# Optimization experiments

Measured on AMD Instinct MI355X. Metric: run time of the kernel, lower is better.

The kernel has to match this reference:

```python
import jax, jax.numpy as jnp
import numpy as np

NC, S, T, F, D, A = 617, 200000, 15, 5, 64, 768
E, EC, L = 1000000, 20000, 2


def setup_inputs():
    key = jax.random.key(0)
    ks = jax.random.split(key, 24)
    f = jnp.float32
    sc = 0.08
    return {
        "company_ts": jax.random.normal(ks[0], (NC, T, F), f),
        "sentence_x": jax.random.normal(ks[1], (S, A), f),
        "company_ids": jnp.arange(NC, dtype=jnp.int32),
        "ei_c2c_src": jax.random.randint(ks[2], (EC,), 0, NC),
        "ei_c2c_dst": jax.random.randint(ks[3], (EC,), 0, NC),
        "ei_s2c_src": jax.random.randint(ks[4], (E,), 0, S),
        "ei_s2c_dst": jax.random.randint(ks[5], (E,), 0, NC),
        "ei_c2s_src": jax.random.randint(ks[6], (E,), 0, NC),
        "ei_c2s_dst": jax.random.randint(ks[7], (E,), 0, S),
        "bn_gamma": jnp.ones((T,), f),
        "bn_beta": jnp.zeros((T,), f),
        "lstm_Wih0": sc * jax.random.normal(ks[8], (4 * D, 1), f),
        "lstm_Whh0": sc * jax.random.normal(ks[9], (4 * D, D), f),
        "lstm_bih0": jnp.zeros((4 * D,), f),
        "lstm_bhh0": jnp.zeros((4 * D,), f),
        "lstm_Wih1": sc * jax.random.normal(ks[10], (4 * D, D), f),
        "lstm_Whh1": sc * jax.random.normal(ks[11], (4 * D, D), f),
        "lstm_bih1": jnp.zeros((4 * D,), f),
        "lstm_bhh1": jnp.zeros((4 * D,), f),
        "fc_W": sc * jax.random.normal(ks[12], (D, D), f),
        "fc_b": jnp.zeros((D,), f),
        "comp_emb": jax.random.normal(ks[13], (NC, D), f),
        "proj_W": sc * jax.random.normal(ks[14], (D, A), f),
        "proj_b": jnp.zeros((D,), f),
        "gin_W": sc * jax.random.normal(ks[15], (L, 3, D, D), f),
        "gin_b": jnp.zeros((L, 3, D), f),
        "gin_a": 0.25 * jnp.ones((L, 3), f),  # PReLU slope, torch default init
        "cls_W": sc * jax.random.normal(ks[16], (2, D), f),
        "cls_b": jnp.zeros((2,), f),
    }


def _lstm_layer(x, Wih, Whh, bih, bhh):
    # x: [N, T, I] -> [N, T, H]; torch gate order i, f, g, o
    N = x.shape[0]
    H = Whh.shape[1]

    def step(carry, xt):
        h, c = carry
        g = xt @ Wih.T + h @ Whh.T + bih + bhh
        i, fg, gg, o = jnp.split(g, 4, axis=-1)
        c = jax.nn.sigmoid(fg) * c + jax.nn.sigmoid(i) * jnp.tanh(gg)
        h = jax.nn.sigmoid(o) * jnp.tanh(c)
        return (h, c), h

    init = (jnp.zeros((N, H), x.dtype), jnp.zeros((N, H), x.dtype))
    _, hs = jax.lax.scan(step, init, jnp.swapaxes(x, 0, 1))
    return jnp.swapaxes(hs, 0, 1)


def _gin(x_src, x_dst, src, dst, n_dst, W, b, a):
    # GINConv(eps=0), nn = Linear + PReLU: prelu(W @ (x_dst + sum_{e->i} x_src[src_e]) + b)
    msg = jax.ops.segment_sum(x_src[src], dst, num_segments=n_dst)
    h = (x_dst + msg) @ W.T + b
    return jnp.where(h >= 0, h, a * h)


def reference(company_ts, sentence_x, company_ids, ei_c2c_src, ei_c2c_dst,
              ei_s2c_src, ei_s2c_dst, ei_c2s_src, ei_c2s_dst,
              bn_gamma, bn_beta, lstm_Wih0, lstm_Whh0, lstm_bih0, lstm_bhh0,
              lstm_Wih1, lstm_Whh1, lstm_bih1, lstm_bhh1, fc_W, fc_b,
              comp_emb, proj_W, proj_b, gin_W, gin_b, gin_a, cls_W, cls_b):
    # LSTM branch on the second-to-last timeseries feature
    ts = company_ts[:, :, -2:-1]                       # [NC, T, 1]
    mean = ts.mean(axis=(0, 2), keepdims=True)         # BatchNorm1d(T), training stats
    var = ts.var(axis=(0, 2), keepdims=True)
    ts = (ts - mean) / jnp.sqrt(var + 1e-5)
    ts = ts * bn_gamma[None, :, None] + bn_beta[None, :, None]
    h = _lstm_layer(ts, lstm_Wih0, lstm_Whh0, lstm_bih0, lstm_bhh0)
    h = _lstm_layer(h, lstm_Wih1, lstm_Whh1, lstm_bih1, lstm_bhh1)
    comp_ts = jax.nn.relu(h[:, -1, :] @ fc_W.T + fc_b)  # [NC, D]

    # node features: company = lstm + embedding; sentence = projected article emb
    comp = comp_ts + comp_emb[company_ids]
    sent = sentence_x @ proj_W.T + proj_b               # [S, D]

    # to_hetero(GConv): per-edge-type GINConv, sum-aggregate over edge types per dst type
    n_comp, n_sent = comp.shape[0], sent.shape[0]
    for l in range(gin_W.shape[0]):
        new_comp = (_gin(comp, comp, ei_c2c_src, ei_c2c_dst, n_comp,
                         gin_W[l, 0], gin_b[l, 0], gin_a[l, 0])
                    + _gin(sent, comp, ei_s2c_src, ei_s2c_dst, n_comp,
                           gin_W[l, 1], gin_b[l, 1], gin_a[l, 1]))
        new_sent = _gin(comp, sent, ei_c2s_src, ei_c2s_dst, n_sent,
                        gin_W[l, 2], gin_b[l, 2], gin_a[l, 2])
        comp, sent = new_comp, new_sent

    return comp @ cls_W.T + cls_b                       # [NC, 2]
```

## Files before the change

kernel.cpp:

```cpp
#include <hip/hip_runtime.h>

#define NCC 617
#define TTT 15
#define FFF 5
#define SSN 200000
#define EEN 1000000
#define ECN 20000
#define CSBLK 196
#define NB2 512
#define EPB2 ((EEN + NB2 - 1) / NB2)
#define ZN (NCC + NCC + SSN + SSN)
#define HALLB ((ECN + EEN + 255) / 256)

typedef unsigned short u16;
typedef unsigned int   u32;

using short8  = __attribute__((ext_vector_type(8))) short;
using f32x4v  = __attribute__((ext_vector_type(4))) float;

__device__ __forceinline__ float bf2f(u16 u){ return __uint_as_float(((u32)u) << 16); }
__device__ __forceinline__ u16 f2bf(float f){
  u32 x = __float_as_uint(f);
  u32 r = (x + 0x7fffu + ((x >> 16) & 1u)) >> 16;
  return (u16)r;
}
__device__ __forceinline__ u32 pk2(float a, float b){ return (u32)f2bf(a) | ((u32)f2bf(b) << 16); }
__device__ __forceinline__ float sigm(float x){ return 1.0f / (1.0f + __expf(-x)); }

__global__ __launch_bounds__(256) void k_zero(int* p, int n){
  int i = blockIdx.x * 256 + threadIdx.x;
  if (i < n) p[i] = 0;
}

__global__ __launch_bounds__(256) void k_histF(const int* __restrict__ s2c_dst, int* __restrict__ blockHist,
                                               const int* __restrict__ c2c_dst, int* __restrict__ cnt_c2c,
                                               const int* __restrict__ c2s_dst, int* __restrict__ cnt_c2s){
  __shared__ int h[NCC];
  int b = blockIdx.x, tid = threadIdx.x;
  if (b < NB2){
    for (int i = tid; i < NCC; i += 256) h[i] = 0;
    __syncthreads();
    int e0 = b * EPB2;
    int e1 = e0 + EPB2; if (e1 > EEN) e1 = EEN;
    for (int e = e0 + tid; e < e1; e += 256) atomicAdd(&h[s2c_dst[e]], 1);
    __syncthreads();
    for (int i = tid; i < NCC; i += 256) blockHist[i * NB2 + b] = h[i];
  } else {
    int i = (b - NB2) * 256 + tid;
    if (i < ECN) atomicAdd(&cnt_c2c[c2c_dst[i]], 1);
    else if (i < ECN + EEN) atomicAdd(&cnt_c2s[c2s_dst[i - ECN]], 1);
  }
}

__global__ __launch_bounds__(1024) void k_scanA(int* __restrict__ blockHist, int* __restrict__ colTotal,
                                                const int* __restrict__ cnt_c2s, int* __restrict__ off_c2s,
                                                int* __restrict__ bsum,
                                                const float* __restrict__ ts, const float* __restrict__ gamma,
                                                const float* __restrict__ beta, float* __restrict__ tsn){
  __shared__ int buf[1024];
  __shared__ float ss[1024], s2[1024];
  int b = blockIdx.x, tid = threadIdx.x;
  if (b < NCC){
    if (tid < 64){
      int lane = tid;
      int base = 0;
      for (int j = 0; j < NB2; j += 64){
        int v = blockHist[b * NB2 + j + lane];
        int orig = v;
        #pragma unroll
        for (int s = 1; s < 64; s <<= 1){
          int t = __shfl_up(v, s, 64);
          if (lane >= s) v += t;
        }
        blockHist[b * NB2 + j + lane] = base + v - orig;
        base += __shfl(v, 63, 64);
      }
      if (lane == 0) colTotal[b] = base;
    }
  } else if (b < NCC + CSBLK) {
    int bb = b - NCC;
    int gi = bb * 1024 + tid;
    int v = (gi < SSN) ? cnt_c2s[gi] : 0;
    buf[tid] = v;
    __syncthreads();
    for (int d = 1; d < 1024; d <<= 1){
      int x = (tid >= d) ? buf[tid - d] : 0;
      __syncthreads();
      buf[tid] += x;
      __syncthreads();
    }
    if (gi < SSN) off_c2s[gi] = buf[tid] - v;
    if (tid == 1023) bsum[bb] = buf[1023];
  } else {
    int t = b - (NCC + CSBLK);
    float a = 0.f, s = 0.f;
    for (int c = tid; c < NCC; c += 1024){
      float v = ts[(c * TTT + t) * FFF + 3];
      a += v; s += v * v;
    }
    ss[tid] = a; s2[tid] = s;
    __syncthreads();
    for (int d = 512; d > 0; d >>= 1){
      if (tid < d){ ss[tid] += ss[tid + d]; s2[tid] += s2[tid + d]; }
      __syncthreads();
    }
    float mean = ss[0] / (float)NCC;
    float var  = s2[0] / (float)NCC - mean * mean;
    float rstd = rsqrtf(var + 1e-5f);
    float g = gamma[t], be = beta[t];
    for (int c = tid; c < NCC; c += 1024){
      float v = ts[(c * TTT + t) * FFF + 3];
      tsn[c * TTT + t] = (v - mean) * rstd * g + be;
    }
  }
}

__global__ __launch_bounds__(1024) void k_scanB(const int* __restrict__ cnt_c2c, int* __restrict__ off_c2c,
                                                const int* __restrict__ colTotal, int* __restrict__ off_s2c,
                                                int* __restrict__ off_c2s, const int* __restrict__ bsum){
  __shared__ int buf[1024];
  __shared__ int sboff[CSBLK + 1];
  int b = blockIdx.x, tid = threadIdx.x;
  if (b == 0){
    for (int pass = 0; pass < 2; ++pass){
      const int* cnt = pass ? colTotal : cnt_c2c;
      int* ofs = pass ? off_s2c : off_c2c;
      int v = (tid < NCC) ? cnt[tid] : 0;
      buf[tid] = v;
      __syncthreads();
      for (int d = 1; d < 1024; d <<= 1){
        int x = (tid >= d) ? buf[tid - d] : 0;
        __syncthreads();
        buf[tid] += x;
        __syncthreads();
      }
      if (tid < NCC) ofs[tid] = (tid == 0) ? 0 : buf[tid - 1];
      if (tid == 0) ofs[NCC] = buf[NCC - 1];
      __syncthreads();
    }
  } else {
    int bb = b - 1;
    int lane = tid & 63;
    if (tid < 64){
      int base = 0;
      for (int j = 0; j < CSBLK; j += 64){
        int idx = j + lane;
        int v = (idx < CSBLK) ? bsum[idx] : 0;
        int orig = v;
        #pragma unroll
        for (int s = 1; s < 64; s <<= 1){
          int t2 = __shfl_up(v, s, 64);
          if (lane >= s) v += t2;
        }
        if (idx < CSBLK) sboff[idx] = base + v - orig;
        base += __shfl(v, 63, 64);
      }
      if (lane == 0) sboff[CSBLK] = base;
    }
    __syncthreads();
    int gi = bb * 1024 + tid;
    if (gi < SSN) off_c2s[gi] += sboff[bb];
    if (bb == 0 && tid == 0) off_c2s[SSN] = sboff[CSBLK];
  }
}

__global__ __launch_bounds__(256) void k_scatF(const int* __restrict__ s2c_src, const int* __restrict__ s2c_dst,
                                               const int* __restrict__ blockHist, const int* __restrict__ off_s2c,
                                               int* __restrict__ bkt_s2c,
                                               const int* __restrict__ c2c_src, const int* __restrict__ c2c_dst,
                                               const int* __restrict__ off_c2c, int* __restrict__ cnt2_c2c,
                                               int* __restrict__ bkt_c2c,
                                               const int* __restrict__ c2s_src, const int* __restrict__ c2s_dst,
                                               const int* __restrict__ off_c2s, int* __restrict__ cnt2_c2s,
                                               int* __restrict__ bkt_c2s){
  __shared__ int cur[NCC];
  int b = blockIdx.x, tid = threadIdx.x;
  if (b < NB2){
    for (int i = tid; i < NCC; i += 256) cur[i] = off_s2c[i] + blockHist[i * NB2 + b];
    __syncthreads();
    int e0 = b * EPB2;
    int e1 = e0 + EPB2; if (e1 > EEN) e1 = EEN;
    for (int e = e0 + tid; e < e1; e += 256){
      int d = s2c_dst[e];
      int p = atomicAdd(&cur[d], 1);
      bkt_s2c[p] = s2c_src[e];
    }
  } else {
    int i = (b - NB2) * 256 + tid;
    if (i < ECN){
      int d = c2c_dst[i]; int p = off_c2c[d] + atomicAdd(&cnt2_c2c[d], 1); bkt_c2c[p] = c2c_src[i];
    } else if (i < ECN + EEN){
      int k = i - ECN;
      int d = c2s_dst[k]; int p = off_c2s[d] + atomicAdd(&cnt2_c2s[d], 1); bkt_c2s[p] = c2s_src[k];
    }
  }
}

__global__ __launch_bounds__(256, 1) void k_lstm01(const float* __restrict__ tsn,
                                                   const float* __restrict__ Wih0, const float* __restrict__ Whh0,
                                                   const float* __restrict__ bih0, const float* __restrict__ bhh0,
                                                   const float* __restrict__ Wih1, const float* __restrict__ Whh1,
                                                   const float* __restrict__ bih1, const float* __restrict__ bhh1,
                                                   const float* __restrict__ fcW, const float* __restrict__ fcb,
                                                   const float* __restrict__ emb, const int* __restrict__ ids,
                                                   float* __restrict__ comp0){
  __shared__ __align__(16) u16 sW0[64 * 64 * 4];
  __shared__ __align__(16) u16 sP1[64 * 64 * 8];
  __shared__ float sWi[256];
  __shared__ float sB0[256];
  int tid = threadIdx.x;
  for (int i = tid; i < 16384; i += 256){
    int k = i >> 8, j = (i >> 2) & 63, g = i & 3;
    sW0[i] = f2bf(Whh0[(g * 64 + j) * 64 + k]);
  }
  for (int i = tid; i < 32768; i += 256){
    int k = i >> 9, j = (i >> 3) & 63, g = i & 7;
    float v = (g < 4) ? Wih1[(g * 64 + j) * 64 + k] : Whh1[((g - 4) * 64 + j) * 64 + k];
    sP1[i] = f2bf(v);
  }
  sWi[tid] = Wih0[tid];
  sB0[tid] = bih0[tid] + bhh0[tid];
  __syncthreads();
  int wave = tid >> 6, lane = tid & 63;
  int c = blockIdx.x * 4 + wave;
  int ci = (c < NCC) ? c : (NCC - 1);
  float wi_i = sWi[lane], wi_f = sWi[64 + lane], wi_g = sWi[128 + lane], wi_o = sWi[192 + lane];
  float b0i = sB0[lane], b0f = sB0[64 + lane], b0g = sB0[128 + lane], b0o = sB0[192 + lane];
  float b1i = bih1[lane]       + bhh1[lane];
  float b1f = bih1[64 + lane]  + bhh1[64 + lane];
  float b1g = bih1[128 + lane] + bhh1[128 + lane];
  float b1o = bih1[192 + lane] + bhh1[192 + lane];
  float h0 = 0.f, c0 = 0.f, h1 = 0.f, c1 = 0.f;
  for (int t = 0; t < TTT; ++t){
    float x = tsn[ci * TTT + t];
    float gi = b0i + x * wi_i, gf = b0f + x * wi_f, gg = b0g + x * wi_g, go = b0o + x * wi_o;
    #pragma unroll 4
    for (int k = 0; k < 64; ++k){
      float hk = __shfl(h0, k, 64);
      ushort4 w = *(const ushort4*)&sW0[(k * 64 + lane) * 4];
      gi += hk * bf2f(w.x); gf += hk * bf2f(w.y);
      gg += hk * bf2f(w.z); go += hk * bf2f(w.w);
    }
    c0 = sigm(gf) * c0 + sigm(gi) * tanhf(gg);
    h0 = sigm(go) * tanhf(c0);
    gi = b1i; gf = b1f; gg = b1g; go = b1o;
    #pragma unroll 4
    for (int k = 0; k < 64; ++k){
      float xk = __shfl(h0, k, 64);
      float hk = __shfl(h1, k, 64);
      short8 wv = *(const short8*)&sP1[(k * 64 + lane) * 8];
      gi += xk * bf2f((u16)wv[0]) + hk * bf2f((u16)wv[4]);
      gf += xk * bf2f((u16)wv[1]) + hk * bf2f((u16)wv[5]);
      gg += xk * bf2f((u16)wv[2]) + hk * bf2f((u16)wv[6]);
      go += xk * bf2f((u16)wv[3]) + hk * bf2f((u16)wv[7]);
    }
    c1 = sigm(gf) * c1 + sigm(gi) * tanhf(gg);
    h1 = sigm(go) * tanhf(c1);
  }
  __syncthreads();
  float* fws = (float*)sW0;
  for (int i = tid; i < 4096; i += 256){
    int d = i >> 6, k = i & 63;
    fws[k * 64 + d] = fcW[i];
  }
  __syncthreads();
  float y = fcb[lane];
  #pragma unroll 4
  for (int k = 0; k < 64; ++k){
    float hk = __shfl(h1, k, 64);
    y += hk * fws[k * 64 + lane];
  }
  y = fmaxf(y, 0.f);
  if (c < NCC) comp0[c * 64 + lane] = y + emb[ids[c] * 64 + lane];
}

__global__ __launch_bounds__(256) void k_projm(const float* __restrict__ A, const float* __restrict__ W,
                                               const float* __restrict__ pb, u16* __restrict__ sent0){
  __shared__ __align__(16) u16 sA[128 * 64];
  __shared__ __align__(16) u16 sB[64 * 64];
  char* sAb = (char*)sA;
  char* sBb = (char*)sB;
  int tid = threadIdx.x;
  int wave = tid >> 6, lane = tid & 63;
  int l15 = lane & 15, lg = lane >> 4;
  int s0 = blockIdx.x * 128;

  int rA = tid >> 1, hA = tid & 1;
  int sA_row = s0 + rA; if (sA_row >= SSN) sA_row = SSN - 1;
  const float* gA0 = &A[(size_t)sA_row * 768 + hA * 32];
  u32 aw_base = (u32)(rA * 128 + hA * 64);
  u32 aw_swz  = (u32)((rA & 7) << 4);
  int nB = tid >> 2, qB = tid & 3;
  const float* gB0 = &W[(size_t)nB * 768 + qB * 16];
  u32 bw_base = (u32)(nB * 128 + qB * 32);
  u32 bw_swz  = (u32)((nB & 7) << 4);

  int arow = wave * 32 + l15;
  u32 ar_swz = (u32)((arow & 7) << 4);
  u32 ar_base = (u32)(arow * 128 + lg * 16);
  u32 br_swz = (u32)((l15 & 7) << 4);
  u32 br_base = (u32)(l15 * 128 + lg * 16);

  f32x4v acc[2][4] = {};

  for (int kc = 0; kc < 12; ++kc){
    __syncthreads();
    {
      const float* g = gA0 + kc * 64;
      #pragma unroll
      for (int q = 0; q < 4; ++q){
        float4 va = ((const float4*)g)[2 * q];
        float4 vb = ((const float4*)g)[2 * q + 1];
        uint4 w;
        w.x = pk2(va.x, va.y); w.y = pk2(va.z, va.w);
        w.z = pk2(vb.x, vb.y); w.w = pk2(vb.z, vb.w);
        *(uint4*)(sAb + ((aw_base + q * 16) ^ aw_swz)) = w;
      }
    }
    {
      const float* g = gB0 + kc * 64;
      #pragma unroll
      for (int q = 0; q < 2; ++q){
        float4 va = ((const float4*)g)[2 * q];
        float4 vb = ((const float4*)g)[2 * q + 1];
        uint4 w;
        w.x = pk2(va.x, va.y); w.y = pk2(va.z, va.w);
        w.z = pk2(vb.x, vb.y); w.w = pk2(vb.z, vb.w);
        *(uint4*)(sBb + ((bw_base + q * 16) ^ bw_swz)) = w;
      }
    }
    __syncthreads();
    #pragma unroll
    for (int ks = 0; ks < 2; ++ks){
      short8 a0 = *(const short8*)(sAb + ((ar_base + 0    + ks * 64) ^ ar_swz));
      short8 a1 = *(const short8*)(sAb + ((ar_base + 2048 + ks * 64) ^ ar_swz));
      short8 b0 = *(const short8*)(sBb + ((br_base + 0    + ks * 64) ^ br_swz));
      short8 b1 = *(const short8*)(sBb + ((br_base + 2048 + ks * 64) ^ br_swz));
      short8 b2 = *(const short8*)(sBb + ((br_base + 4096 + ks * 64) ^ br_swz));
      short8 b3 = *(const short8*)(sBb + ((br_base + 6144 + ks * 64) ^ br_swz));
      acc[0][0] = __builtin_amdgcn_mfma_f32_16x16x32_bf16(a0, b0, acc[0][0], 0, 0, 0);
      acc[0][1] = __builtin_amdgcn_mfma_f32_16x16x32_bf16(a0, b1, acc[0][1], 0, 0, 0);
      acc[0][2] = __builtin_amdgcn_mfma_f32_16x16x32_bf16(a0, b2, acc[0][2], 0, 0, 0);
      acc[0][3] = __builtin_amdgcn_mfma_f32_16x16x32_bf16(a0, b3, acc[0][3], 0, 0, 0);
      acc[1][0] = __builtin_amdgcn_mfma_f32_16x16x32_bf16(a1, b0, acc[1][0], 0, 0, 0);
      acc[1][1] = __builtin_amdgcn_mfma_f32_16x16x32_bf16(a1, b1, acc[1][1], 0, 0, 0);
      acc[1][2] = __builtin_amdgcn_mfma_f32_16x16x32_bf16(a1, b2, acc[1][2], 0, 0, 0);
      acc[1][3] = __builtin_amdgcn_mfma_f32_16x16x32_bf16(a1, b3, acc[1][3], 0, 0, 0);
    }
  }

  float bias[4];
  #pragma unroll
  for (int nt = 0; nt < 4; ++nt) bias[nt] = pb[nt * 16 + l15];
  #pragma unroll
  for (int mt = 0; mt < 2; ++mt){
    #pragma unroll
    for (int j = 0; j < 4; ++j){
      int s = s0 + wave * 32 + mt * 16 + lg * 4 + j;
      if (s < SSN){
        #pragma unroll
        for (int nt = 0; nt < 4; ++nt)
          sent0[(size_t)s * 64 + nt * 16 + l15] = f2bf(acc[mt][nt][j] + bias[nt]);
      }
    }
  }
}

__global__ __launch_bounds__(256) void k_sgin(const u16* __restrict__ sentIn, const float* __restrict__ compIn,
                                              const int* __restrict__ ofs, const int* __restrict__ bkt,
                                              const float* __restrict__ W, const float* __restrict__ b,
                                              const float* __restrict__ aP, u16* __restrict__ sentOut){
  __shared__ __align__(16) u16 sX[64 * 64];
  __shared__ __align__(16) u16 sW[64 * 64];
  __shared__ int eb[512];
  __shared__ int sofs[65];
  char* sXb = (char*)sX;
  char* sWb = (char*)sW;
  int tid = threadIdx.x;
  {
    int n = tid >> 2, q = tid & 3;
    const float* g = &W[n * 64 + q * 16];
    u32 wbase = (u32)(n * 128 + q * 32);
    u32 wswz  = (u32)((n & 7) << 4);
    #pragma unroll
    for (int hh = 0; hh < 2; ++hh){
      float4 va = ((const float4*)g)[2 * hh];
      float4 vb = ((const float4*)g)[2 * hh + 1];
      uint4 w;
      w.x = pk2(va.x, va.y); w.y = pk2(va.z, va.w);
      w.z = pk2(vb.x, vb.y); w.w = pk2(vb.z, vb.w);
      *(uint4*)(sWb + ((wbase + hh * 16) ^ wswz)) = w;
    }
  }
  int sBase = blockIdx.x * 64;
  if (tid < 65) sofs[tid] = ofs[sBase + tid];
  __syncthreads();
  int E0 = sofs[0];
  int tot = sofs[64] - E0;
  int staged = tot < 512 ? tot : 512;
  for (int i = tid; i < staged; i += 256) eb[i] = bkt[E0 + i];
  __syncthreads();
  int wave = tid >> 6, lane = tid & 63;
  for (int q = 0; q < 16; ++q){
    int sL = wave * 16 + q;
    int s = sBase + sL;
    float acc = bf2f(sentIn[(size_t)s * 64 + lane]);
    int e0 = sofs[sL], e1 = sofs[sL + 1];
    for (int e = e0; e < e1; ++e){
      int r = e - E0;
      int src = (r < 512) ? eb[r] : bkt[e];
      acc += compIn[src * 64 + lane];
    }
    *(u16*)(sXb + (((u32)(sL * 128 + lane * 2)) ^ ((u32)((sL & 7) << 4)))) = f2bf(acc);
  }
  __syncthreads();
  int l15 = lane & 15, lg = lane >> 4;
  int arow = wave * 16 + l15;
  u32 ar_swz = (u32)((arow & 7) << 4);
  u32 br_swz = (u32)((l15 & 7) << 4);
  f32x4v acc4[4] = {};
  #pragma unroll
  for (int ks = 0; ks < 2; ++ks){
    short8 a0 = *(const short8*)(sXb + (((u32)(arow * 128 + ks * 64 + lg * 16)) ^ ar_swz));
    #pragma unroll
    for (int nt = 0; nt < 4; ++nt){
      short8 b0 = *(const short8*)(sWb + (((u32)((nt * 16 + l15) * 128 + ks * 64 + lg * 16)) ^ br_swz));
      acc4[nt] = __builtin_amdgcn_mfma_f32_16x16x32_bf16(a0, b0, acc4[nt], 0, 0, 0);
    }
  }
  float alpha = *aP;
  #pragma unroll
  for (int nt = 0; nt < 4; ++nt){
    float bb = b[nt * 16 + l15];
    #pragma unroll
    for (int j = 0; j < 4; ++j){
      int srow = sBase + wave * 16 + lg * 4 + j;
      float h = acc4[nt][j] + bb;
      h = (h >= 0.f) ? h : alpha * h;
      sentOut[(size_t)srow * 64 + nt * 16 + l15] = f2bf(h);
    }
  }
}

__global__ __launch_bounds__(1024) void k_cgin(const float* __restrict__ compIn, const u16* __restrict__ sentIn,
                                               const int* __restrict__ ofsA, const int* __restrict__ bktA,
                                               const int* __restrict__ ofsB, const int* __restrict__ bktB,
                                               const float* __restrict__ Wa, const float* __restrict__ ba, const float* aaP,
                                               const float* __restrict__ Wb, const float* __restrict__ bb, const float* abP,
                                               float* __restrict__ compOut,
                                               const float* __restrict__ clsW, const float* __restrict__ clsb,
                                               float* __restrict__ outp){
  __shared__ __align__(16) float Wat[64 * 68];
  __shared__ __align__(16) float Wbt[64 * 68];
  __shared__ int eidx[2048];
  __shared__ float part[16][2][64];
  __shared__ float xa[64], xb[64], outab[128];
  int tid = threadIdx.x;
  for (int i = tid; i < 4096; i += 1024){
    int j = i >> 6, k = i & 63;
    Wat[k * 68 + j] = Wa[i];
    Wbt[k * 68 + j] = Wb[i];
  }
  int wave = tid >> 6, lane = tid & 63;
  int c = blockIdx.x;
  float accA = 0.f, accB = 0.f;
  int a0 = ofsA[c], a1 = ofsA[c + 1];
  for (int base = a0; base < a1; base += 2048){
    int cnt = a1 - base; if (cnt > 2048) cnt = 2048;
    __syncthreads();
    for (int i = tid; i < cnt; i += 1024) eidx[i] = bktA[base + i];
    __syncthreads();
    for (int i = wave; i < cnt; i += 16) accA += compIn[eidx[i] * 64 + lane];
  }
  int b0 = ofsB[c], b1 = ofsB[c + 1];
  for (int base = b0; base < b1; base += 2048){
    int cnt = b1 - base; if (cnt > 2048) cnt = 2048;
    __syncthreads();
    for (int i = tid; i < cnt; i += 1024) eidx[i] = bktB[base + i];
    __syncthreads();
    #pragma unroll 4
    for (int i = wave; i < cnt; i += 16) accB += bf2f(sentIn[(size_t)eidx[i] * 64 + lane]);
  }
  part[wave][0][lane] = accA;
  part[wave][1][lane] = accB;
  __syncthreads();
  if (tid < 128){
    int l = tid & 63, which = tid >> 6;
    float m = 0.f;
    #pragma unroll
    for (int w = 0; w < 16; ++w) m += part[w][which][l];
    float ci = compIn[c * 64 + l];
    if (which == 0) xa[l] = ci + m; else xb[l] = ci + m;
  }
  __syncthreads();
  if (tid < 128){
    int j = tid & 63;
    const float* X  = (tid < 64) ? xa : xb;
    const float* Wt = (tid < 64) ? Wat : Wbt;
    float acc = (tid < 64) ? ba[j] : bb[j];
    #pragma unroll 4
    for (int k = 0; k < 64; ++k) acc += X[k] * Wt[k * 68 + j];
    float al = (tid < 64) ? *aaP : *abP;
    outab[tid] = (acc >= 0.f) ? acc : al * acc;
  }
  __syncthreads();
  if (clsW){
    if (tid < 64) xa[tid] = outab[tid] + outab[64 + tid];
    __syncthreads();
    if (tid < 128){
      int j = tid >> 6;
      float p = xa[lane] * clsW[j * 64 + lane];
      #pragma unroll
      for (int s = 32; s > 0; s >>= 1) p += __shfl_down(p, s, 64);
      if (lane == 0) outp[c * 2 + j] = p + clsb[j];
    }
  } else {
    if (tid < 64) compOut[c * 64 + tid] = outab[tid] + outab[64 + tid];
  }
}

extern "C" void kernel_launch(void* const* d_in, const int* in_sizes, int n_in,
                              void* d_out, int out_size, void* d_ws, size_t ws_size,
                              hipStream_t stream) {
  (void)in_sizes; (void)n_in; (void)out_size; (void)ws_size;
  const float* company_ts = (const float*)d_in[0];
  const float* sentence_x = (const float*)d_in[1];
  const int*   company_ids = (const int*)d_in[2];
  const int*   c2c_src = (const int*)d_in[3];
  const int*   c2c_dst = (const int*)d_in[4];
  const int*   s2c_src = (const int*)d_in[5];
  const int*   s2c_dst = (const int*)d_in[6];
  const int*   c2s_src = (const int*)d_in[7];
  const int*   c2s_dst = (const int*)d_in[8];
  const float* bn_gamma = (const float*)d_in[9];
  const float* bn_beta  = (const float*)d_in[10];
  const float* Wih0 = (const float*)d_in[11];
  const float* Whh0 = (const float*)d_in[12];
  const float* bih0 = (const float*)d_in[13];
  const float* bhh0 = (const float*)d_in[14];
  const float* Wih1 = (const float*)d_in[15];
  const float* Whh1 = (const float*)d_in[16];
  const float* bih1 = (const float*)d_in[17];
  const float* bhh1 = (const float*)d_in[18];
  const float* fc_W = (const float*)d_in[19];
  const float* fc_b = (const float*)d_in[20];
  const float* comp_emb = (const float*)d_in[21];
  const float* proj_W = (const float*)d_in[22];
  const float* proj_b = (const float*)d_in[23];
  const float* gin_W = (const float*)d_in[24];
  const float* gin_b = (const float*)d_in[25];
  const float* gin_a = (const float*)d_in[26];
  const float* cls_W = (const float*)d_in[27];
  const float* cls_b = (const float*)d_in[28];
  float* outp = (float*)d_out;

  char* ws = (char*)d_ws;
  size_t off = 0;
  auto alloc = [&](size_t bytes)->char* {
    char* r = ws + off;
    off += (bytes + 255) & ~(size_t)255;
    return r;
  };
  float* ts_norm = (float*)alloc((size_t)NCC * TTT * 4);
  float* comp0   = (float*)alloc((size_t)NCC * 64 * 4);
  float* comp1   = (float*)alloc((size_t)NCC * 64 * 4);
  u16*   sent0   = (u16*)alloc((size_t)SSN * 64 * 2);
  int*   blockHist = (int*)alloc((size_t)NCC * NB2 * 4);
  int*   colTotal  = (int*)alloc((size_t)NCC * 4);
  int*   cnt_c2c  = (int*)alloc((size_t)ZN * 4);
  int*   cnt2_c2c = cnt_c2c + NCC;
  int*   cnt_c2s  = cnt2_c2c + NCC;
  int*   cnt2_c2s = cnt_c2s + SSN;
  int*   off_c2c = (int*)alloc((size_t)(NCC + 1) * 4);
  int*   off_s2c = (int*)alloc((size_t)(NCC + 1) * 4);
  int*   off_c2s = (int*)alloc((size_t)(SSN + 1) * 4);
  int*   bkt_c2c = (int*)alloc((size_t)ECN * 4);
  int*   bkt_s2c = (int*)alloc((size_t)EEN * 4);
  int*   bkt_c2s = (int*)alloc((size_t)EEN * 4);
  int*   bsum    = (int*)alloc(256 * 4);

  k_zero<<<(ZN + 255) / 256, 256, 0, stream>>>(cnt_c2c, ZN);
  k_histF<<<NB2 + HALLB, 256, 0, stream>>>(s2c_dst, blockHist, c2c_dst, cnt_c2c, c2s_dst, cnt_c2s);
  k_scanA<<<NCC + CSBLK + TTT, 1024, 0, stream>>>(blockHist, colTotal, cnt_c2s, off_c2s, bsum,
                                                  company_ts, bn_gamma, bn_beta, ts_norm);
  k_scanB<<<1 + CSBLK, 1024, 0, stream>>>(cnt_c2c, off_c2c, colTotal, off_s2c, off_c2s, bsum);
  k_scatF<<<NB2 + HALLB, 256, 0, stream>>>(s2c_src, s2c_dst, blockHist, off_s2c, bkt_s2c,
                                           c2c_src, c2c_dst, off_c2c, cnt2_c2c, bkt_c2c,
                                           c2s_src, c2s_dst, off_c2s, cnt2_c2s, bkt_c2s);

  k_lstm01<<<(NCC + 3) / 4, 256, 0, stream>>>(ts_norm, Wih0, Whh0, bih0, bhh0,
                                              Wih1, Whh1, bih1, bhh1,
                                              fc_W, fc_b, comp_emb, company_ids, comp0);

  k_projm<<<(SSN + 127) / 128, 256, 0, stream>>>(sentence_x, proj_W, proj_b, sent0);

  k_cgin<<<NCC, 1024, 0, stream>>>(comp0, sent0,
                                   off_c2c, bkt_c2c, off_s2c, bkt_s2c,
                                   gin_W + 0 * 4096, gin_b + 0 * 64, gin_a + 0,
                                   gin_W + 1 * 4096, gin_b + 1 * 64, gin_a + 1,
                                   comp1, nullptr, nullptr, nullptr);
  k_sgin<<<SSN / 64, 256, 0, stream>>>(sent0, comp0, off_c2s, bkt_c2s,
                                       gin_W + 2 * 4096, gin_b + 2 * 64, gin_a + 2,
                                       sent0 );

  k_cgin<<<NCC, 1024, 0, stream>>>(comp1, sent0,
                                   off_c2c, bkt_c2c, off_s2c, bkt_s2c,
                                   gin_W + 3 * 4096, gin_b + 3 * 64, gin_a + 3,
                                   gin_W + 4 * 4096, gin_b + 4 * 64, gin_a + 4,
                                   nullptr, cls_W, cls_b, outp);
}
```

Measured before the change: 565.3 us.

## Fuse layer-0 company and sentence GIN into one launch with separate output buffer

Merges the layer-0 company GIN and sentence GIN kernels into a single launch, where the first blocks handle companies and the rest handle sentences in 256-row tiles of 1024 threads. Sentence output now goes to a new sent1 buffer instead of overwriting sent0 in place, so both branches can run concurrently and read the same inputs. The final layer gets a specialised kernel without the nullptr branch, and the gather loops get larger unroll factors. The aim is to overlap the short company work with the large sentence gather and drop one kernel launch. The cost is extra workspace and larger blocks in the sentence path.

```diff
diff --git a/kernel.cpp b/kernel.cpp
--- a/kernel.cpp
+++ b/kernel.cpp
@@ -11,6 +11,7 @@
 #define EPB2 ((EEN + NB2 - 1) / NB2)
 #define ZN (NCC + NCC + SSN + SSN)
 #define HALLB ((ECN + EEN + 255) / 256)
+#define SGB 782
 
 typedef unsigned short u16;
 typedef unsigned int   u32;
@@ -366,90 +367,156 @@
   }
 }
 
-__global__ __launch_bounds__(256) void k_sgin(const u16* __restrict__ sentIn, const float* __restrict__ compIn,
-                                              const int* __restrict__ ofs, const int* __restrict__ bkt,
-                                              const float* __restrict__ W, const float* __restrict__ b,
-                                              const float* __restrict__ aP, u16* __restrict__ sentOut){
-  __shared__ __align__(16) u16 sX[64 * 64];
-  __shared__ __align__(16) u16 sW[64 * 64];
-  __shared__ int eb[512];
-  __shared__ int sofs[65];
-  char* sXb = (char*)sX;
-  char* sWb = (char*)sW;
+__global__ __launch_bounds__(1024) void k_gin0(const float* __restrict__ compIn, const u16* __restrict__ sentIn,
+                                               const int* __restrict__ ofsA, const int* __restrict__ bktA,
+                                               const int* __restrict__ ofsB, const int* __restrict__ bktB,
+                                               const int* __restrict__ ofsS, const int* __restrict__ bktS,
+                                               const float* __restrict__ gin_W, const float* __restrict__ gin_b,
+                                               const float* __restrict__ gin_a,
+                                               float* __restrict__ compOut, u16* __restrict__ sentOut){
+  __shared__ __align__(16) char smem[52224];
   int tid = threadIdx.x;
-  {
-    int n = tid >> 2, q = tid & 3;
-    const float* g = &W[n * 64 + q * 16];
-    u32 wbase = (u32)(n * 128 + q * 32);
-    u32 wswz  = (u32)((n & 7) << 4);
+  int wave = tid >> 6, lane = tid & 63;
+  int b = blockIdx.x;
+  if (b < NCC){
+    float* Wat  = (float*)smem;
+    float* Wbt  = Wat + 64 * 68;
+    int*   eidx = (int*)(Wbt + 64 * 68);
+    float* part = (float*)(eidx + 2048);
+    float* xa   = part + 2048;
+    float* xb   = xa + 64;
+    float* outab = xb + 64;
+    const float* Wa = gin_W + 0 * 4096;
+    const float* Wb = gin_W + 1 * 4096;
+    for (int i = tid; i < 4096; i += 1024){
+      int j = i >> 6, k = i & 63;
+      Wat[k * 68 + j] = Wa[i];
+      Wbt[k * 68 + j] = Wb[i];
+    }
+    int c = b;
+    float accA = 0.f, accB = 0.f;
+    int a0 = ofsA[c], a1 = ofsA[c + 1];
+    for (int base = a0; base < a1; base += 2048){
+      int cnt = a1 - base; if (cnt > 2048) cnt = 2048;
+      __syncthreads();
+      for (int i = tid; i < cnt; i += 1024) eidx[i] = bktA[base + i];
+      __syncthreads();
+      #pragma unroll 4
+      for (int i = wave; i < cnt; i += 16) accA += compIn[eidx[i] * 64 + lane];
+    }
+    int b0 = ofsB[c], b1 = ofsB[c + 1];
+    for (int base = b0; base < b1; base += 2048){
+      int cnt = b1 - base; if (cnt > 2048) cnt = 2048;
+      __syncthreads();
+      for (int i = tid; i < cnt; i += 1024) eidx[i] = bktB[base + i];
+      __syncthreads();
+      #pragma unroll 8
+      for (int i = wave; i < cnt; i += 16) accB += bf2f(sentIn[(size_t)eidx[i] * 64 + lane]);
+    }
+    part[(wave * 2 + 0) * 64 + lane] = accA;
+    part[(wave * 2 + 1) * 64 + lane] = accB;
+    __syncthreads();
+    if (tid < 128){
+      int l = tid & 63, which = tid >> 6;
+      float m = 0.f;
+      #pragma unroll
+      for (int w = 0; w < 16; ++w) m += part[(w * 2 + which) * 64 + l];
+      float ci = compIn[c * 64 + l];
+      if (which == 0) xa[l] = ci + m; else xb[l] = ci + m;
+    }
+    __syncthreads();
+    if (tid < 128){
+      int j = tid & 63;
+      const float* X  = (tid < 64) ? xa : xb;
+      const float* Wt = (tid < 64) ? Wat : Wbt;
+      float acc = (tid < 64) ? gin_b[j] : gin_b[64 + j];
+      #pragma unroll 4
+      for (int k = 0; k < 64; ++k) acc += X[k] * Wt[k * 68 + j];
+      float al = (tid < 64) ? gin_a[0] : gin_a[1];
+      outab[tid] = (acc >= 0.f) ? acc : al * acc;
+    }
+    __syncthreads();
+    if (tid < 64) compOut[c * 64 + tid] = outab[tid] + outab[64 + tid];
+  } else {
+    u16* sX   = (u16*)smem;
+    u16* sW   = sX + 16384;
+    int* eb   = (int*)(sW + 4096);
+    int* sofs = eb + 2048;
+    char* sXb = (char*)sX;
+    char* sWb = (char*)sW;
+    const float* W = gin_W + 2 * 4096;
+    const float* bi = gin_b + 128;
+    {
+      int n = tid >> 4, q = tid & 15;
+      float4 v = *(const float4*)&W[n * 64 + q * 4];
+      uint2 w;
+      w.x = pk2(v.x, v.y); w.y = pk2(v.z, v.w);
+      *(uint2*)(sWb + (((u32)(n * 128 + q * 8)) ^ ((u32)((n & 7) << 4)))) = w;
+    }
+    int sBase = (b - NCC) * 256;
+    if (tid < 257){
+      int idx = sBase + tid; if (idx > SSN) idx = SSN;
+      sofs[tid] = ofsS[idx];
+    }
+    __syncthreads();
+    int E0 = sofs[0];
+    int tot = sofs[256] - E0;
+    int staged = tot < 2048 ? tot : 2048;
+    for (int i = tid; i < staged; i += 1024) eb[i] = bktS[E0 + i];
+    __syncthreads();
+    for (int q = 0; q < 16; ++q){
+      int sL = wave * 16 + q;
+      int s = sBase + sL;
+      if (s < SSN){
+        float acc = bf2f(sentIn[(size_t)s * 64 + lane]);
+        int e0 = sofs[sL], e1 = sofs[sL + 1];
+        for (int e = e0; e < e1; ++e){
+          int r = e - E0;
+          int src = (r < 2048) ? eb[r] : bktS[e];
+          acc += compIn[src * 64 + lane];
+        }
+        *(u16*)(sXb + (((u32)(sL * 128 + lane * 2)) ^ ((u32)((sL & 7) << 4)))) = f2bf(acc);
+      }
+    }
+    __syncthreads();
+    int l15 = lane & 15, lg = lane >> 4;
+    int arow = wave * 16 + l15;
+    u32 ar_swz = (u32)((arow & 7) << 4);
+    u32 br_swz = (u32)((l15 & 7) << 4);
+    f32x4v acc4[4] = {};
     #pragma unroll
-    for (int hh = 0; hh < 2; ++hh){
-      float4 va = ((const float4*)g)[2 * hh];
-      float4 vb = ((const float4*)g)[2 * hh + 1];
-      uint4 w;
-      w.x = pk2(va.x, va.y); w.y = pk2(va.z, va.w);
-      w.z = pk2(vb.x, vb.y); w.w = pk2(vb.z, vb.w);
-      *(uint4*)(sWb + ((wbase + hh * 16) ^ wswz)) = w;
-    }
-  }
-  int sBase = blockIdx.x * 64;
-  if (tid < 65) sofs[tid] = ofs[sBase + tid];
-  __syncthreads();
-  int E0 = sofs[0];
-  int tot = sofs[64] - E0;
-  int staged = tot < 512 ? tot : 512;
-  for (int i = tid; i < staged; i += 256) eb[i] = bkt[E0 + i];
-  __syncthreads();
-  int wave = tid >> 6, lane = tid & 63;
-  for (int q = 0; q < 16; ++q){
-    int sL = wave * 16 + q;
-    int s = sBase + sL;
-    float acc = bf2f(sentIn[(size_t)s * 64 + lane]);
-    int e0 = sofs[sL], e1 = sofs[sL + 1];
-    for (int e = e0; e < e1; ++e){
-      int r = e - E0;
-      int src = (r < 512) ? eb[r] : bkt[e];
-      acc += compIn[src * 64 + lane];
-    }
-    *(u16*)(sXb + (((u32)(sL * 128 + lane * 2)) ^ ((u32)((sL & 7) << 4)))) = f2bf(acc);
-  }
-  __syncthreads();
-  int l15 = lane & 15, lg = lane >> 4;
-  int arow = wave * 16 + l15;
-  u32 ar_swz = (u32)((arow & 7) << 4);
-  u32 br_swz = (u32)((l15 & 7) << 4);
-  f32x4v acc4[4] = {};
-  #pragma unroll
-  for (int ks = 0; ks < 2; ++ks){
-    short8 a0 = *(const short8*)(sXb + (((u32)(arow * 128 + ks * 64 + lg * 16)) ^ ar_swz));
+    for (int ks = 0; ks < 2; ++ks){
+      short8 a0 = *(const short8*)(sXb + (((u32)(arow * 128 + ks * 64 + lg * 16)) ^ ar_swz));
+      #pragma unroll
+      for (int nt = 0; nt < 4; ++nt){
+        short8 b0 = *(const short8*)(sWb + (((u32)((nt * 16 + l15) * 128 + ks * 64 + lg * 16)) ^ br_swz));
+        acc4[nt] = __builtin_amdgcn_mfma_f32_16x16x32_bf16(a0, b0, acc4[nt], 0, 0, 0);
+      }
+    }
+    float alpha = gin_a[2];
     #pragma unroll
     for (int nt = 0; nt < 4; ++nt){
-      short8 b0 = *(const short8*)(sWb + (((u32)((nt * 16 + l15) * 128 + ks * 64 + lg * 16)) ^ br_swz));
-      acc4[nt] = __builtin_amdgcn_mfma_f32_16x16x32_bf16(a0, b0, acc4[nt], 0, 0, 0);
-    }
-  }
-  float alpha = *aP;
-  #pragma unroll
-  for (int nt = 0; nt < 4; ++nt){
-    float bb = b[nt * 16 + l15];
-    #pragma unroll
-    for (int j = 0; j < 4; ++j){
-      int srow = sBase + wave * 16 + lg * 4 + j;
-      float h = acc4[nt][j] + bb;
-      h = (h >= 0.f) ? h : alpha * h;
-      sentOut[(size_t)srow * 64 + nt * 16 + l15] = f2bf(h);
-    }
-  }
-}
-
-__global__ __launch_bounds__(1024) void k_cgin(const float* __restrict__ compIn, const u16* __restrict__ sentIn,
-                                               const int* __restrict__ ofsA, const int* __restrict__ bktA,
-                                               const int* __restrict__ ofsB, const int* __restrict__ bktB,
-                                               const float* __restrict__ Wa, const float* __restrict__ ba, const float* aaP,
-                                               const float* __restrict__ Wb, const float* __restrict__ bb, const float* abP,
-                                               float* __restrict__ compOut,
-                                               const float* __restrict__ clsW, const float* __restrict__ clsb,
-                                               float* __restrict__ outp){
+      float bb = bi[nt * 16 + l15];
+      #pragma unroll
+      for (int j = 0; j < 4; ++j){
+        int srow = sBase + wave * 16 + lg * 4 + j;
+        if (srow < SSN){
+          float h = acc4[nt][j] + bb;
+          h = (h >= 0.f) ? h : alpha * h;
+          sentOut[(size_t)srow * 64 + nt * 16 + l15] = f2bf(h);
+        }
+      }
+    }
+  }
+}
+
+__global__ __launch_bounds__(1024) void k_cgin1(const float* __restrict__ compIn, const u16* __restrict__ sentIn,
+                                                const int* __restrict__ ofsA, const int* __restrict__ bktA,
+                                                const int* __restrict__ ofsB, const int* __restrict__ bktB,
+                                                const float* __restrict__ Wa, const float* __restrict__ ba, const float* aaP,
+                                                const float* __restrict__ Wb, const float* __restrict__ bb, const float* abP,
+                                                const float* __restrict__ clsW, const float* __restrict__ clsb,
+                                                float* __restrict__ outp){
   __shared__ __align__(16) float Wat[64 * 68];
   __shared__ __align__(16) float Wbt[64 * 68];
   __shared__ int eidx[2048];
@@ -470,6 +537,7 @@
     __syncthreads();
     for (int i = tid; i < cnt; i += 1024) eidx[i] = bktA[base + i];
     __syncthreads();
+    #pragma unroll 4
     for (int i = wave; i < cnt; i += 16) accA += compIn[eidx[i] * 64 + lane];
   }
   int b0 = ofsB[c], b1 = ofsB[c + 1];
@@ -478,7 +546,7 @@
     __syncthreads();
     for (int i = tid; i < cnt; i += 1024) eidx[i] = bktB[base + i];
     __syncthreads();
-    #pragma unroll 4
+    #pragma unroll 8
     for (int i = wave; i < cnt; i += 16) accB += bf2f(sentIn[(size_t)eidx[i] * 64 + lane]);
   }
   part[wave][0][lane] = accA;
@@ -504,18 +572,14 @@
     outab[tid] = (acc >= 0.f) ? acc : al * acc;
   }
   __syncthreads();
-  if (clsW){
-    if (tid < 64) xa[tid] = outab[tid] + outab[64 + tid];
-    __syncthreads();
-    if (tid < 128){
-      int j = tid >> 6;
-      float p = xa[lane] * clsW[j * 64 + lane];
-      #pragma unroll
-      for (int s = 32; s > 0; s >>= 1) p += __shfl_down(p, s, 64);
-      if (lane == 0) outp[c * 2 + j] = p + clsb[j];
-    }
-  } else {
-    if (tid < 64) compOut[c * 64 + tid] = outab[tid] + outab[64 + tid];
+  if (tid < 64) xa[tid] = outab[tid] + outab[64 + tid];
+  __syncthreads();
+  if (tid < 128){
+    int j = tid >> 6;
+    float p = xa[lane] * clsW[j * 64 + lane];
+    #pragma unroll
+    for (int s = 32; s > 0; s >>= 1) p += __shfl_down(p, s, 64);
+    if (lane == 0) outp[c * 2 + j] = p + clsb[j];
   }
 }
 
@@ -565,6 +629,7 @@
   float* comp0   = (float*)alloc((size_t)NCC * 64 * 4);
   float* comp1   = (float*)alloc((size_t)NCC * 64 * 4);
   u16*   sent0   = (u16*)alloc((size_t)SSN * 64 * 2);
+  u16*   sent1   = (u16*)alloc((size_t)SSN * 64 * 2);
   int*   blockHist = (int*)alloc((size_t)NCC * NB2 * 4);
   int*   colTotal  = (int*)alloc((size_t)NCC * 4);
   int*   cnt_c2c  = (int*)alloc((size_t)ZN * 4);
@@ -594,18 +659,15 @@
 
   k_projm<<<(SSN + 127) / 128, 256, 0, stream>>>(sentence_x, proj_W, proj_b, sent0);
 
-  k_cgin<<<NCC, 1024, 0, stream>>>(comp0, sent0,
-                                   off_c2c, bkt_c2c, off_s2c, bkt_s2c,
-                                   gin_W + 0 * 4096, gin_b + 0 * 64, gin_a + 0,
-                                   gin_W + 1 * 4096, gin_b + 1 * 64, gin_a + 1,
-                                   comp1, nullptr, nullptr, nullptr);
-  k_sgin<<<SSN / 64, 256, 0, stream>>>(sent0, comp0, off_c2s, bkt_c2s,
-                                       gin_W + 2 * 4096, gin_b + 2 * 64, gin_a + 2,
-                                       sent0 );
-
-  k_cgin<<<NCC, 1024, 0, stream>>>(comp1, sent0,
-                                   off_c2c, bkt_c2c, off_s2c, bkt_s2c,
-                                   gin_W + 3 * 4096, gin_b + 3 * 64, gin_a + 3,
-                                   gin_W + 4 * 4096, gin_b + 4 * 64, gin_a + 4,
-                                   nullptr, cls_W, cls_b, outp);
-}
+  k_gin0<<<NCC + SGB, 1024, 0, stream>>>(comp0, sent0,
+                                         off_c2c, bkt_c2c, off_s2c, bkt_s2c,
+                                         off_c2s, bkt_c2s,
+                                         gin_W, gin_b, gin_a,
+                                         comp1, sent1);
+
+  k_cgin1<<<NCC, 1024, 0, stream>>>(comp1, sent1,
+                                    off_c2c, bkt_c2c, off_s2c, bkt_s2c,
+                                    gin_W + 3 * 4096, gin_b + 3 * 64, gin_a + 3,
+                                    gin_W + 4 * 4096, gin_b + 4 * 64, gin_a + 4,
+                                    cls_W, cls_b, outp);
+}
```

New measurement: 552.5 us, median of 2. 2.3% less time.
